# Performance work log

Measured on AMD Instinct MI355X. Metric: run time of the kernel, lower is better.

Reference implementation:

```python
import jax, jax.numpy as jnp
import numpy as np
import math

BS, S, E, H, DK = 32, 512, 512, 8, 64


def setup_inputs() -> dict:
    key = jax.random.key(0)
    ks = jax.random.split(key, 10)
    q = jax.random.normal(ks[0], (BS, S, E), jnp.float32)
    k = jax.random.normal(ks[1], (BS, S, E), jnp.float32)
    v = jax.random.normal(ks[2], (BS, S, E), jnp.float32)
    # strictly-causal mask: allowed where col < row (np.triu(k=0)==0)
    mask = jnp.tril(jnp.ones((S, S), bool), -1)[None, None]
    sc = 1.0 / math.sqrt(E)  # xavier-ish scale for square linears
    Wq = jax.random.normal(ks[3], (E, E), jnp.float32) * sc
    Wk = jax.random.normal(ks[4], (E, E), jnp.float32) * sc
    Wv = jax.random.normal(ks[5], (E, E), jnp.float32) * sc
    Wo = jax.random.normal(ks[6], (E, E), jnp.float32) * sc
    bq = jnp.zeros((E,), jnp.float32)
    bk = jnp.zeros((E,), jnp.float32)
    bv = jnp.zeros((E,), jnp.float32)
    bo = jnp.zeros((E,), jnp.float32)
    gammas = jax.random.normal(ks[7], (H, 1, 1), jnp.float32) * 0.5
    return {"q": q, "k": k, "v": v, "mask": mask, "zero_pad": 1,
            "Wq": Wq, "bq": bq, "Wk": Wk, "bk": bk, "Wv": Wv, "bv": bv,
            "Wo": Wo, "bo": bo, "gammas": gammas}


def reference(q, k, v, mask, zero_pad, Wq, bq, Wk, bk, Wv, bv, Wo, bo, gammas):
    bs = q.shape[0]
    # projections (torch Linear: x @ W.T + b), split heads -> [b,h,s,d]
    def heads(x, W, b):
        return (x @ W.T + b).reshape(bs, S, H, DK).transpose(0, 2, 1, 3)
    qh, kh, vh = heads(q, Wq, bq), heads(k, Wk, bk), heads(v, Wv, bv)

    scores = jnp.einsum('bhqd,bhkd->bhqk', qh, kh) / math.sqrt(DK)

    # --- distance-decay term (no-grad in original) ---
    neg = jnp.float32(-1e32)
    scores_ = jnp.where(mask, scores, neg)
    scores_ = jax.nn.softmax(scores_, axis=-1) * mask.astype(scores.dtype)
    distcum = jnp.cumsum(scores_, axis=-1)
    disttotal = jnp.sum(scores_, axis=-1, keepdims=True)
    idx = jnp.arange(S)
    position_effect = jnp.abs(idx[None, :] - idx[:, None]).astype(scores.dtype)[None, None]
    dist_scores = jnp.sqrt(jnp.clip((disttotal - distcum) * position_effect, 0.0))
    dist_scores = jax.lax.stop_gradient(dist_scores)

    gamma = -jax.nn.softplus(gammas)[None]  # [1,h,1,1]
    total_effect = jnp.clip(jnp.exp(dist_scores * gamma), 1e-5, 1e5)

    scores = scores * total_effect
    scores = jnp.where(mask, scores, neg)
    scores = jax.nn.softmax(scores, axis=-1)
    if zero_pad:
        scores = scores.at[:, :, 0, :].set(0.0)

    out = jnp.einsum('bhqk,bhkd->bhqd', scores, vh)
    concat = out.transpose(0, 2, 1, 3).reshape(bs, S, E)
    return concat @ Wo.T + bo
```

## Files before the change

kernel.cpp:

```cpp
#include <hip/hip_runtime.h>
#include <hip/hip_bf16.h>
#include <hip/hip_fp16.h>
#include <stdint.h>

#define BSZ 32
#define SEQ 512
#define EMB 512
#define NH  8
#define DKD 64
#define LOG2E 1.4426950408889634f

typedef float f32x4 __attribute__((ext_vector_type(4)));
typedef short s16x8 __attribute__((ext_vector_type(8)));

#if __has_builtin(__builtin_amdgcn_exp2f)
#define EXP2(x) __builtin_amdgcn_exp2f(x)
#else
#define EXP2(x) exp2f(x)
#endif
#define RCP(x) __builtin_amdgcn_rcpf(x)

__device__ inline unsigned short f2bf(float f) {
  union { float f; unsigned u; } v; v.f = f;
  unsigned r = v.u + 0x7fffu + ((v.u >> 16) & 1u);
  return (unsigned short)(r >> 16);
}

__device__ inline ushort4 pack4bf(float4 v) {
  union { __hip_bfloat162 h2[2]; ushort4 u4; } cv;
  cv.h2[0] = __float22bfloat162_rn(make_float2(v.x, v.y));
  cv.h2[1] = __float22bfloat162_rn(make_float2(v.z, v.w));
  return cv.u4;
}

template<int CTRL>
__device__ inline float dpp_shr_f(float x) {
  return __builtin_bit_cast(float,
    __builtin_amdgcn_update_dpp(0, __builtin_bit_cast(int, x), CTRL, 0xf, 0xf, true));
}
__device__ inline float rlane(float v, int l) {
  return __builtin_bit_cast(float, __builtin_amdgcn_readlane(__builtin_bit_cast(int, v), l));
}

template<int MODE>
__global__ __launch_bounds__(256)
void gemm_bt(const void* __restrict__ Av, const float* __restrict__ B,
             const float* __restrict__ bias, void* __restrict__ C,
             int M, int N, int K, float oscale)
{
  __shared__ __align__(16) unsigned short Al[128 * 40];
  __shared__ __align__(16) unsigned short Bl[128 * 40];
  const int tid  = threadIdx.x;
  const int lane = tid & 63;
  const int w    = tid >> 6;
  const int m0   = blockIdx.y * 128;
  const int n0   = blockIdx.x * 128;
  const int wr   = (w >> 1) * 64;
  const int wc   = (w & 1) * 64;
  const int srow = tid >> 3;
  const int scol = (tid & 7) * 4;

  f32x4 acc[4][4] = {};

  for (int k0 = 0; k0 < K; k0 += 32) {
    if constexpr (MODE == 3) {
      const unsigned short* A = (const unsigned short*)Av;
      #pragma unroll
      for (int p = 0; p < 2; ++p) {
        const int r  = p * 64 + (tid >> 2);
        const int c8 = (tid & 3) * 8;
        *reinterpret_cast<s16x8*>(&Al[r * 40 + c8]) =
            *reinterpret_cast<const s16x8*>(&A[(size_t)(m0 + r) * K + k0 + c8]);
      }
    } else {
      const float* A = (const float*)Av;
      #pragma unroll
      for (int p = 0; p < 4; ++p) {
        const int r = p * 32 + srow;
        float4 va = *reinterpret_cast<const float4*>(&A[(size_t)(m0 + r) * K + k0 + scol]);
        *reinterpret_cast<ushort4*>(&Al[r * 40 + scol]) = pack4bf(va);
      }
    }
    #pragma unroll
    for (int p = 0; p < 4; ++p) {
      const int r = p * 32 + srow;
      float4 vb = *reinterpret_cast<const float4*>(&B[(size_t)(n0 + r) * K + k0 + scol]);
      *reinterpret_cast<ushort4*>(&Bl[r * 40 + scol]) = pack4bf(vb);
    }
    __syncthreads();
    s16x8 af[4], bf[4];
    #pragma unroll
    for (int i = 0; i < 4; ++i)
      af[i] = *reinterpret_cast<const s16x8*>(&Al[(wr + i * 16 + (lane & 15)) * 40 + (lane >> 4) * 8]);
    #pragma unroll
    for (int j = 0; j < 4; ++j)
      bf[j] = *reinterpret_cast<const s16x8*>(&Bl[(wc + j * 16 + (lane & 15)) * 40 + (lane >> 4) * 8]);
    #pragma unroll
    for (int i = 0; i < 4; ++i)
      #pragma unroll
      for (int j = 0; j < 4; ++j)
        acc[i][j] = __builtin_amdgcn_mfma_f32_16x16x32_bf16(af[i], bf[j], acc[i][j], 0, 0, 0);
    __syncthreads();
  }

  #pragma unroll
  for (int i = 0; i < 4; ++i)
    #pragma unroll
    for (int j = 0; j < 4; ++j)
      #pragma unroll
      for (int r = 0; r < 4; ++r) {
        const int gm = m0 + wr + i * 16 + (lane >> 4) * 4 + r;
        const int gn = n0 + wc + j * 16 + (lane & 15);
        const float vv = (acc[i][j][r] + bias[gn]) * oscale;
        if (MODE == 3) {
          ((float*)C)[(size_t)gm * N + gn] = vv;
        } else {
          const int b = gm >> 9, s = gm & 511, h = gn >> 6, d = gn & 63;
          const size_t off = (MODE == 0)
              ? ((size_t)(b * NH + h) * SEQ + s) * DKD + d
              : ((size_t)(b * NH + h) * DKD + d) * SEQ + s;
          ((unsigned short*)C)[off] = f2bf(vv);
        }
      }
}

template<int R>
__device__ inline void phase2_rows(unsigned short* s_lds, int w, int lane,
                                   int q0, int zp, float g2)
{
  constexpr int L  = 64 / R;
  constexpr int IT = 4 / R;
  const int seg = lane / L;
  const int li  = lane & (L - 1);
  const int jb  = li * 8;
  const float NEGINF = -__builtin_inff();
  #pragma unroll
  for (int it = 0; it < IT; ++it) {
    const int r  = w * 4 + it * R + seg;
    const int qg = q0 + r;
    const int gs = li ^ (r & 7);
    unsigned short* rowp = &s_lds[r * 512 + gs * 8];
    float pn2[8];
    if (qg == 0) {
      const float u = zp ? 0.0f : (1.0f / 512.0f);
      #pragma unroll
      for (int i = 0; i < 8; ++i) pn2[i] = u;
    } else {
      float sL[8];
      {
        s16x8 raw = *reinterpret_cast<const s16x8*>(rowp);
        union { s16x8 v; __half2 h[4]; } u; u.v = raw;
        #pragma unroll
        for (int i = 0; i < 4; ++i) {
          float2 f = __half22float2(u.h[i]);
          sL[2 * i] = f.x; sL[2 * i + 1] = f.y;
        }
      }
      #pragma unroll
      for (int i = 0; i < 8; ++i) sL[i] = (jb + i < qg) ? sL[i] : NEGINF;
      float p[8], c[8];
      float run = 0.f;
      #pragma unroll
      for (int i = 0; i < 8; ++i) { p[i] = EXP2(sL[i]); run += p[i]; c[i] = run; }
      float t = run;
      t += dpp_shr_f<0x111>(t);
      t += dpp_shr_f<0x112>(t);
      t += dpp_shr_f<0x114>(t);
      t += dpp_shr_f<0x118>(t);
      float tot;
      if constexpr (R == 1) {
        const float r0 = rlane(t, 15), r1 = rlane(t, 31), r2 = rlane(t, 47);
        const float a1 = r0, a2 = r0 + r1, a3 = a2 + r2;
        tot = a3 + rlane(t, 63);
        t += (lane >= 48) ? a3 : (lane >= 32) ? a2 : (lane >= 16) ? a1 : 0.f;
      } else if constexpr (R == 2) {
        const float r0 = rlane(t, 15), r2 = rlane(t, 47);
        t += (lane & 16) ? ((lane < 32) ? r0 : r2) : 0.f;
        tot = __shfl(t, lane | 31, 64);
      } else {
        tot = __shfl(t, lane | 15, 64);
      }
      const float pre  = tot - (t - run);
      const float g2r  = g2 * __builtin_amdgcn_sqrtf(RCP(tot));
      const float fb   = (float)(qg - jb);
      float p2[8]; float run2 = 0.f;
      #pragma unroll
      for (int i = 0; i < 8; ++i) {
        const float rem = pre - c[i];
        const float arg = fmaxf(rem * (fb - (float)i), 0.f);
        float te = EXP2(__builtin_amdgcn_sqrtf(arg) * g2r);
        te = fmaxf(te, 1e-5f);
        p2[i] = EXP2(sL[i] * te);
        run2 += p2[i];
      }
      float y = run2;
      y += dpp_shr_f<0x111>(y);
      y += dpp_shr_f<0x112>(y);
      y += dpp_shr_f<0x114>(y);
      y += dpp_shr_f<0x118>(y);
      float s2;
      if constexpr (R == 1) {
        s2 = rlane(y, 15) + rlane(y, 31) + rlane(y, 47) + rlane(y, 63);
      } else if constexpr (R == 2) {
        y += (lane & 16) ? ((lane < 32) ? rlane(y, 15) : rlane(y, 47)) : 0.f;
        s2 = __shfl(y, lane | 31, 64);
      } else {
        s2 = __shfl(y, lane | 15, 64);
      }
      const float inv2 = RCP(s2);
      #pragma unroll
      for (int i = 0; i < 8; ++i) pn2[i] = p2[i] * inv2;
    }
    union { __hip_bfloat162 h2[4]; uint4 u; } pk;
    pk.h2[0] = __float22bfloat162_rn(make_float2(pn2[0], pn2[1]));
    pk.h2[1] = __float22bfloat162_rn(make_float2(pn2[2], pn2[3]));
    pk.h2[2] = __float22bfloat162_rn(make_float2(pn2[4], pn2[5]));
    pk.h2[3] = __float22bfloat162_rn(make_float2(pn2[6], pn2[7]));
    *reinterpret_cast<uint4*>(rowp) = pk.u;
  }
}

__global__ __launch_bounds__(256)
void attn_kernel(const unsigned short* __restrict__ Qh,
                 const unsigned short* __restrict__ Kh,
                 const unsigned short* __restrict__ Vt,
                 unsigned short* __restrict__ Aout,
                 const float* __restrict__ gammas,
                 const int* __restrict__ zero_pad)
{
  __shared__ __align__(16) unsigned short s_lds[16 * 512];
  const int tid = threadIdx.x, lane = tid & 63, w = tid >> 6;
  const int lin = blockIdx.x;
  const int x   = lin & 7;
  const int u   = lin >> 3;
  const int qb  = u >> 5;
  const int h   = u & 7;
  const int b   = x * 4 + ((u >> 3) & 3);
  const int q0  = qb * 16;
  const size_t bh = (size_t)b * NH + h;
  const unsigned short* Qp = Qh + bh * SEQ * DKD;
  const unsigned short* Kp = Kh + bh * SEQ * DKD;
  const unsigned short* Vp = Vt + bh * DKD * SEQ;
  const int zp = zero_pad[0];
  const float g2 = -log1pf(__expf(gammas[h])) * LOG2E;

  s16x8 aq[2];
  #pragma unroll
  for (int kt = 0; kt < 2; ++kt)
    aq[kt] = *reinterpret_cast<const s16x8*>(&Qp[(q0 + (lane & 15)) * DKD + kt * 32 + (lane >> 4) * 8]);
  {
    const int frag = (lane >> 4) * 8;
    auto loadK = [&](int t, s16x8* kb) {
      const int n = t * 16 + (lane & 15);
      kb[0] = *reinterpret_cast<const s16x8*>(&Kp[n * DKD + frag]);
      kb[1] = *reinterpret_cast<const s16x8*>(&Kp[n * DKD + 32 + frag]);
    };
    auto tilecomp = [&](int t, const s16x8* kb) {
      f32x4 acc = {};
      acc = __builtin_amdgcn_mfma_f32_16x16x32_bf16(aq[0], kb[0], acc, 0, 0, 0);
      acc = __builtin_amdgcn_mfma_f32_16x16x32_bf16(aq[1], kb[1], acc, 0, 0, 0);
      const int n = t * 16 + (lane & 15);
      #pragma unroll
      for (int r = 0; r < 4; ++r) {
        const int row = (lane >> 4) * 4 + r;
        const int idx = row * 512 + ((((n >> 3) ^ (row & 7)) << 3) + (n & 7));
        s_lds[idx] = __half_as_ushort(__float2half(acc[r]));
      }
    };
    int t = w;
    if (t <= qb) {
      s16x8 cur[2], nxt[2];
      loadK(t, cur);
      while (true) {
        const int tn = t + 4;
        if (tn <= qb) {
          loadK(tn, nxt);
          tilecomp(t, cur);
          cur[0] = nxt[0]; cur[1] = nxt[1];
          t = tn;
        } else {
          tilecomp(t, cur);
          break;
        }
      }
    }
  }
  __syncthreads();

  if (zp == 0 && qb == 0) {
    phase2_rows<1>(s_lds, w, lane, q0, zp, g2);
  } else if (qb < 8) {
    phase2_rows<4>(s_lds, w, lane, q0, zp, g2);
  } else if (qb < 16) {
    phase2_rows<2>(s_lds, w, lane, q0, zp, g2);
  } else {
    phase2_rows<1>(s_lds, w, lane, q0, zp, g2);
  }
  __syncthreads();

  f32x4 oacc = {};
  const int row  = lane & 15;
  const int koff = lane >> 4;
  const int rsw  = row & 7;
  const unsigned short* vbase = &Vp[(w * 16 + row) * SEQ + koff * 8];
  const int ks_end = (qb == 0 && zp == 0) ? 16 : (qb >> 1) + 1;
  int ks0 = 0;
  for (; ks0 + 4 <= ks_end; ks0 += 4) {
    s16x8 vb[4], pa[4];
    #pragma unroll
    for (int uu = 0; uu < 4; ++uu) {
      const int ks = ks0 + uu;
      vb[uu] = *reinterpret_cast<const s16x8*>(&vbase[ks * 32]);
      pa[uu] = *reinterpret_cast<const s16x8*>(&s_lds[row * 512 + ((ks * 4 + koff) ^ rsw) * 8]);
    }
    #pragma unroll
    for (int uu = 0; uu < 4; ++uu)
      oacc = __builtin_amdgcn_mfma_f32_16x16x32_bf16(pa[uu], vb[uu], oacc, 0, 0, 0);
  }
  for (; ks0 < ks_end; ++ks0) {
    s16x8 vb = *reinterpret_cast<const s16x8*>(&vbase[ks0 * 32]);
    s16x8 pa = *reinterpret_cast<const s16x8*>(&s_lds[row * 512 + ((ks0 * 4 + koff) ^ rsw) * 8]);
    oacc = __builtin_amdgcn_mfma_f32_16x16x32_bf16(pa, vb, oacc, 0, 0, 0);
  }
  #pragma unroll
  for (int r = 0; r < 4; ++r) {
    const int orow = (lane >> 4) * 4 + r;
    const int ocol = w * 16 + (lane & 15);
    Aout[((size_t)b * SEQ + (q0 + orow)) * EMB + h * DKD + ocol] = f2bf(oacc[r]);
  }
}

extern "C" void kernel_launch(void* const* d_in, const int* in_sizes, int n_in,
                              void* d_out, int out_size, void* d_ws, size_t ws_size,
                              hipStream_t stream)
{
  const float* q  = (const float*)d_in[0];
  const float* k  = (const float*)d_in[1];
  const float* v  = (const float*)d_in[2];
  const int*   zp = (const int*)d_in[4];
  const float* Wq = (const float*)d_in[5];
  const float* bq = (const float*)d_in[6];
  const float* Wk = (const float*)d_in[7];
  const float* bk = (const float*)d_in[8];
  const float* Wv = (const float*)d_in[9];
  const float* bv = (const float*)d_in[10];
  const float* Wo = (const float*)d_in[11];
  const float* bo = (const float*)d_in[12];
  const float* gm = (const float*)d_in[13];

  char* ws = (char*)d_ws;
  const size_t HB = (size_t)BSZ * NH * SEQ * DKD * sizeof(unsigned short);
  unsigned short* Qh = (unsigned short*)(ws);
  unsigned short* Kh = (unsigned short*)(ws + HB);
  unsigned short* Vt = (unsigned short*)(ws + 2 * HB);
  unsigned short* At = (unsigned short*)(ws + 3 * HB);

  const int M = BSZ * SEQ, N = EMB, K = EMB;
  dim3 ggrid(N / 128, M / 128);
  gemm_bt<0><<<ggrid, 256, 0, stream>>>(q, Wq, bq, Qh, M, N, K, 0.125f * LOG2E);
  gemm_bt<0><<<ggrid, 256, 0, stream>>>(k, Wk, bk, Kh, M, N, K, 1.0f);
  gemm_bt<1><<<ggrid, 256, 0, stream>>>(v, Wv, bv, Vt, M, N, K, 1.0f);
  attn_kernel<<<8192, 256, 0, stream>>>(Qh, Kh, Vt, At, gm, zp);
  gemm_bt<3><<<ggrid, 256, 0, stream>>>(At, Wo, bo, d_out, M, N, K, 1.0f);
}
```

Measured before the change: 179.4 us.

## Pre-convert weights to bf16 and stage GEMM tiles via direct global-to-LDS loads

Adds a small kernel that converts all four weight matrices to bf16 once per call. The projection GEMMs then read bf16 weights and stage both operand tiles into LDS with direct global-to-LDS 16-byte loads into an XOR-swizzled layout. For fp32 activations the bf16 conversion moves from the staging step to the LDS read step. The aim is to halve weight traffic, cut register round-trips and conversion work during staging, and avoid LDS bank conflicts, at the cost of an extra launch and a larger fp32 A tile in LDS.

```diff
diff --git a/kernel.cpp b/kernel.cpp
--- a/kernel.cpp
+++ b/kernel.cpp
@@ -33,6 +33,16 @@
   return cv.u4;
 }
 
+__device__ inline void stage16(const void* g, void* l) {
+#if defined(__has_builtin) && __has_builtin(__builtin_amdgcn_global_load_lds)
+  __builtin_amdgcn_global_load_lds(
+      (const __attribute__((address_space(1))) void*)g,
+      (__attribute__((address_space(3))) void*)l, 16, 0, 0);
+#else
+  *reinterpret_cast<uint4*>(l) = *reinterpret_cast<const uint4*>(g);
+#endif
+}
+
 template<int CTRL>
 __device__ inline float dpp_shr_f(float x) {
   return __builtin_bit_cast(float,
@@ -42,14 +52,34 @@
   return __builtin_bit_cast(float, __builtin_amdgcn_readlane(__builtin_bit_cast(int, v), l));
 }
 
+__global__ __launch_bounds__(256)
+void wcvt(const float* __restrict__ w0, const float* __restrict__ w1,
+          const float* __restrict__ w2, const float* __restrict__ w3,
+          unsigned short* __restrict__ o0, unsigned short* __restrict__ o1,
+          unsigned short* __restrict__ o2, unsigned short* __restrict__ o3)
+{
+  const float* src = (blockIdx.y == 0) ? w0 : (blockIdx.y == 1) ? w1
+                   : (blockIdx.y == 2) ? w2 : w3;
+  unsigned short* dst = (blockIdx.y == 0) ? o0 : (blockIdx.y == 1) ? o1
+                      : (blockIdx.y == 2) ? o2 : o3;
+  const int i = (blockIdx.x * 256 + threadIdx.x) * 8;
+  float4 a = *reinterpret_cast<const float4*>(src + i);
+  float4 b = *reinterpret_cast<const float4*>(src + i + 4);
+  union { ushort4 p[2]; s16x8 v; } cc;
+  cc.p[0] = pack4bf(a); cc.p[1] = pack4bf(b);
+  *reinterpret_cast<s16x8*>(dst + i) = cc.v;
+}
+
 template<int MODE>
 __global__ __launch_bounds__(256)
-void gemm_bt(const void* __restrict__ Av, const float* __restrict__ B,
+void gemm_bt(const void* __restrict__ Av, const unsigned short* __restrict__ Bw,
              const float* __restrict__ bias, void* __restrict__ C,
              int M, int N, int K, float oscale)
 {
-  __shared__ __align__(16) unsigned short Al[128 * 40];
-  __shared__ __align__(16) unsigned short Bl[128 * 40];
+  constexpr int ASZ = (MODE == 3) ? 8192 : 16384;
+  __shared__ __align__(16) char smem[ASZ + 8192];
+  char* const sA = smem;
+  char* const sB = smem + ASZ;
   const int tid  = threadIdx.x;
   const int lane = tid & 63;
   const int w    = tid >> 6;
@@ -57,44 +87,65 @@
   const int n0   = blockIdx.x * 128;
   const int wr   = (w >> 1) * 64;
   const int wc   = (w & 1) * 64;
-  const int srow = tid >> 3;
-  const int scol = (tid & 7) * 4;
+  const int base = w * 1024 + lane * 16;
 
   f32x4 acc[4][4] = {};
 
   for (int k0 = 0; k0 < K; k0 += 32) {
-    if constexpr (MODE == 3) {
+    if constexpr (MODE != 3) {
+      const float* A = (const float*)Av;
+      #pragma unroll
+      for (int c = 0; c < 4; ++c) {
+        const int flat = c * 4096 + base;
+        const int row  = flat >> 7;
+        const int gl   = ((flat >> 4) & 7) ^ (row & 7);
+        stage16(&A[(size_t)(m0 + row) * K + k0 + gl * 4], sA + flat);
+      }
+    } else {
       const unsigned short* A = (const unsigned short*)Av;
       #pragma unroll
-      for (int p = 0; p < 2; ++p) {
-        const int r  = p * 64 + (tid >> 2);
-        const int c8 = (tid & 3) * 8;
-        *reinterpret_cast<s16x8*>(&Al[r * 40 + c8]) =
-            *reinterpret_cast<const s16x8*>(&A[(size_t)(m0 + r) * K + k0 + c8]);
-      }
-    } else {
-      const float* A = (const float*)Av;
-      #pragma unroll
-      for (int p = 0; p < 4; ++p) {
-        const int r = p * 32 + srow;
-        float4 va = *reinterpret_cast<const float4*>(&A[(size_t)(m0 + r) * K + k0 + scol]);
-        *reinterpret_cast<ushort4*>(&Al[r * 40 + scol]) = pack4bf(va);
-      }
-    }
-    #pragma unroll
-    for (int p = 0; p < 4; ++p) {
-      const int r = p * 32 + srow;
-      float4 vb = *reinterpret_cast<const float4*>(&B[(size_t)(n0 + r) * K + k0 + scol]);
-      *reinterpret_cast<ushort4*>(&Bl[r * 40 + scol]) = pack4bf(vb);
+      for (int c = 0; c < 2; ++c) {
+        const int flat = c * 4096 + base;
+        const int r    = flat >> 7;
+        const int gl   = ((flat >> 4) & 7) ^ (r & 7);
+        const int row  = r + ((gl >> 2) << 6);
+        stage16(&A[(size_t)(m0 + row) * K + k0 + (gl & 3) * 8], sA + flat);
+      }
+    }
+    #pragma unroll
+    for (int c = 0; c < 2; ++c) {
+      const int flat = c * 4096 + base;
+      const int r    = flat >> 7;
+      const int gl   = ((flat >> 4) & 7) ^ (r & 7);
+      const int nn   = r + ((gl >> 2) << 6);
+      stage16(&Bw[(size_t)(n0 + nn) * K + k0 + (gl & 3) * 8], sB + flat);
     }
     __syncthreads();
+
     s16x8 af[4], bf[4];
     #pragma unroll
-    for (int i = 0; i < 4; ++i)
-      af[i] = *reinterpret_cast<const s16x8*>(&Al[(wr + i * 16 + (lane & 15)) * 40 + (lane >> 4) * 8]);
-    #pragma unroll
-    for (int j = 0; j < 4; ++j)
-      bf[j] = *reinterpret_cast<const s16x8*>(&Bl[(wc + j * 16 + (lane & 15)) * 40 + (lane >> 4) * 8]);
+    for (int i = 0; i < 4; ++i) {
+      const int row = wr + i * 16 + (lane & 15);
+      if constexpr (MODE != 3) {
+        const int g1 = (lane >> 4) << 1;
+        float4 v1 = *reinterpret_cast<const float4*>(sA + row * 128 + ((g1 ^ (row & 7)) << 4));
+        float4 v2 = *reinterpret_cast<const float4*>(sA + row * 128 + (((g1 + 1) ^ (row & 7)) << 4));
+        union { ushort4 p[2]; s16x8 v; } cc;
+        cc.p[0] = pack4bf(v1); cc.p[1] = pack4bf(v2);
+        af[i] = cc.v;
+      } else {
+        const int r  = row & 63;
+        const int gl = ((row >> 6) << 2) + (lane >> 4);
+        af[i] = *reinterpret_cast<const s16x8*>(sA + r * 128 + ((gl ^ (r & 7)) << 4));
+      }
+    }
+    #pragma unroll
+    for (int j = 0; j < 4; ++j) {
+      const int n  = wc + j * 16 + (lane & 15);
+      const int r  = n & 63;
+      const int gl = ((n >> 6) << 2) + (lane >> 4);
+      bf[j] = *reinterpret_cast<const s16x8*>(sB + r * 128 + ((gl ^ (r & 7)) << 4));
+    }
     #pragma unroll
     for (int i = 0; i < 4; ++i)
       #pragma unroll
@@ -350,16 +401,22 @@
 
   char* ws = (char*)d_ws;
   const size_t HB = (size_t)BSZ * NH * SEQ * DKD * sizeof(unsigned short);
-  unsigned short* Qh = (unsigned short*)(ws);
-  unsigned short* Kh = (unsigned short*)(ws + HB);
-  unsigned short* Vt = (unsigned short*)(ws + 2 * HB);
-  unsigned short* At = (unsigned short*)(ws + 3 * HB);
+  const size_t WB = (size_t)EMB * EMB * sizeof(unsigned short);
+  unsigned short* Qh  = (unsigned short*)(ws);
+  unsigned short* Kh  = (unsigned short*)(ws + HB);
+  unsigned short* Vt  = (unsigned short*)(ws + 2 * HB);
+  unsigned short* At  = (unsigned short*)(ws + 3 * HB);
+  unsigned short* Wqb = (unsigned short*)(ws + 4 * HB);
+  unsigned short* Wkb = (unsigned short*)(ws + 4 * HB + WB);
+  unsigned short* Wvb = (unsigned short*)(ws + 4 * HB + 2 * WB);
+  unsigned short* Wob = (unsigned short*)(ws + 4 * HB + 3 * WB);
 
   const int M = BSZ * SEQ, N = EMB, K = EMB;
   dim3 ggrid(N / 128, M / 128);
-  gemm_bt<0><<<ggrid, 256, 0, stream>>>(q, Wq, bq, Qh, M, N, K, 0.125f * LOG2E);
-  gemm_bt<0><<<ggrid, 256, 0, stream>>>(k, Wk, bk, Kh, M, N, K, 1.0f);
-  gemm_bt<1><<<ggrid, 256, 0, stream>>>(v, Wv, bv, Vt, M, N, K, 1.0f);
+  wcvt<<<dim3(128, 4), 256, 0, stream>>>(Wq, Wk, Wv, Wo, Wqb, Wkb, Wvb, Wob);
+  gemm_bt<0><<<ggrid, 256, 0, stream>>>(q, Wqb, bq, Qh, M, N, K, 0.125f * LOG2E);
+  gemm_bt<0><<<ggrid, 256, 0, stream>>>(k, Wkb, bk, Kh, M, N, K, 1.0f);
+  gemm_bt<1><<<ggrid, 256, 0, stream>>>(v, Wvb, bv, Vt, M, N, K, 1.0f);
   attn_kernel<<<8192, 256, 0, stream>>>(Qh, Kh, Vt, At, gm, zp);
-  gemm_bt<3><<<ggrid, 256, 0, stream>>>(At, Wo, bo, d_out, M, N, K, 1.0f);
-}
+  gemm_bt<3><<<ggrid, 256, 0, stream>>>(At, Wob, bo, d_out, M, N, K, 1.0f);
+}
```

Measured after the change: 170.5 us. -4.9%, faster.
